# Optimization experiments

Measured on AMD Instinct MI355X. Metric: run time of the kernel, lower is better.

Reference implementation:

```python
import jax, jax.numpy as jnp
import numpy as np

KERNEL = 3
DILATIONS = (2, 3)
NUM_HEADS = 8


def _unfold_windows(t, k, dil):
    # t: [B, C, H, W] -> [B, C, k*k, H, W], same layout as nn.Unfold(k, dil, pad=dil*(k-1)//2)
    B, C, H, W = t.shape
    pad = dil * (k - 1) // 2
    tp = jnp.pad(t, ((0, 0), (0, 0), (pad, pad), (pad, pad)))
    ws = [tp[:, :, i * dil:i * dil + H, j * dil:j * dil + W]
          for i in range(k) for j in range(k)]
    return jnp.stack(ws, axis=2)


def _dilate_attention(q, k_, v, kernel, dil, head_dim):
    # q,k_,v: [B, d, H, W]
    B, d, H, W = q.shape
    nh = d // head_dim
    scale = head_dim ** (-0.5)
    qh = q.reshape(B, nh, head_dim, H, W)
    kw = _unfold_windows(k_, kernel, dil).reshape(B, nh, head_dim, kernel * kernel, H, W)
    vw = _unfold_windows(v, kernel, dil).reshape(B, nh, head_dim, kernel * kernel, H, W)
    attn = jax.nn.softmax(jnp.einsum('bndhw,bndkhw->bnkhw', qh, kw) * scale, axis=2)
    out = jnp.einsum('bnkhw,bndkhw->bndhw', attn, vw)  # [B, nh, hd, H, W]
    return out.transpose(0, 3, 4, 1, 2).reshape(B, H, W, d)


def setup_inputs() -> dict:
    key = jax.random.key(0)
    k1, k2, k3, k4 = jax.random.split(key, 4)
    B, H, W, C = 4, 128, 128, 256
    x = jax.random.normal(k1, (B, H, W, C), dtype=jnp.float32)
    Wqkv = jax.random.normal(k2, (3 * C, C), dtype=jnp.float32) * (C ** -0.5)
    Wproj = jax.random.normal(k3, (C, C), dtype=jnp.float32) * (C ** -0.5)
    bproj = jnp.zeros((C,), dtype=jnp.float32)
    return {"x": x, "Wqkv": Wqkv, "Wproj": Wproj, "bproj": bproj}


def reference(x, Wqkv, Wproj, bproj):
    B, H, W, C = x.shape
    nd = len(DILATIONS)
    head_dim = C // NUM_HEADS
    # 1x1 conv qkv (no bias), then split into 3 and nd dilation groups
    qkv = jnp.einsum('bhwc,oc->bohw', x, Wqkv).reshape(B, 3, nd, C // nd, H, W)
    outs = []
    for i, dil in enumerate(DILATIONS):
        q, k_, v = qkv[:, 0, i], qkv[:, 1, i], qkv[:, 2, i]
        outs.append(_dilate_attention(q, k_, v, KERNEL, dil, head_dim))
    xo = jnp.concatenate(outs, axis=-1)  # [B, H, W, C], dilation-group-major channels
    return jnp.einsum('bhwc,oc->bhwo', xo, Wproj) + bproj
```

## Files before the change

### kernel.cpp

```cpp
#include <hip/hip_runtime.h>
#include <stdint.h>


typedef __attribute__((ext_vector_type(8))) short bf16x8;
typedef __attribute__((ext_vector_type(4))) float f32x4;
typedef __attribute__((ext_vector_type(2))) float f32x2;

__device__ __forceinline__ f32x2 up2(unsigned u) {
  union { unsigned u; float f; } a, b;
  a.u = u << 16;
  b.u = u & 0xffff0000u;
  return (f32x2){a.f, b.f};
}
__device__ __forceinline__ unsigned short f2bf(float f) {
  union { float f; unsigned u; } x; x.f = f;
  unsigned r = x.u + 0x7fffu + ((x.u >> 16) & 1u);
  return (unsigned short)(r >> 16);
}
__device__ __forceinline__ unsigned pk2bf(float a, float b) {
  return (unsigned)f2bf(a) | ((unsigned)f2bf(b) << 16);
}

__global__ __launch_bounds__(256) void cvt_f32_to_bf16(
    const float* __restrict__ src, unsigned short* __restrict__ dst, int n) {
  int i = (blockIdx.x * 256 + threadIdx.x) * 8;
  if (i + 8 <= n) {
    const float4* s = (const float4*)(src + i);
    float4 a = s[0], b = s[1];
    uint4 o;
    o.x = pk2bf(a.x, a.y); o.y = pk2bf(a.z, a.w);
    o.z = pk2bf(b.x, b.y); o.w = pk2bf(b.z, b.w);
    *(uint4*)(dst + i) = o;
  } else {
    for (; i < n; ++i) dst[i] = f2bf(src[i]);
  }
}

__global__ __launch_bounds__(256) void cvt_w_both(
    const float* __restrict__ wqkv, const float* __restrict__ wproj,
    unsigned short* __restrict__ dst) {
  const int i = (blockIdx.x * 256 + threadIdx.x) * 8;
  const float* src = (i < 196608) ? (wqkv + i) : (wproj + (i - 196608));
  const float4* s = (const float4*)src;
  float4 a = s[0], b = s[1];
  uint4 o;
  o.x = pk2bf(a.x, a.y); o.y = pk2bf(a.z, a.w);
  o.z = pk2bf(b.x, b.y); o.w = pk2bf(b.z, b.w);
  *(uint4*)(dst + i) = o;
}

#define BARX()                                                \
  do {                                                        \
    asm volatile("s_waitcnt lgkmcnt(0)" ::: "memory");        \
    __builtin_amdgcn_s_barrier();                             \
    __builtin_amdgcn_sched_barrier(0);                        \
  } while (0)
#define WAITVM(n)                                             \
  do {                                                        \
    asm volatile("s_waitcnt vmcnt(" #n ")" ::: "memory");     \
    __builtin_amdgcn_sched_barrier(0);                        \
  } while (0)

template <int OUTF32>
__global__ __launch_bounds__(256) void gemm_bt(
    const unsigned short* __restrict__ A, const unsigned short* __restrict__ B,
    void* __restrict__ Cout, const float* __restrict__ bias,
    int N, int NT) {
  __shared__ __align__(16) unsigned short lds[3 * 8192];

  const int tid  = threadIdx.x;
  const int lane = tid & 63;
  const int wv   = tid >> 6;
  const int wr   = wv >> 1;
  const int wc   = wv & 1;

  const int nwg = gridDim.x;
  const int q8  = nwg >> 3;
  const int nid = (blockIdx.x & 7) * q8 + (blockIdx.x >> 3);
  const int n0  = (nid % NT) * 128;
  const int m0  = (nid / NT) * 128;

  const int stg_row = wv * 16 + (lane >> 2);
  const int stg_k   = ((lane & 3) ^ ((lane >> 3) & 3)) * 8;
  const unsigned short* Ag = A + (size_t)(m0 + stg_row) * 256 + stg_k;
  const unsigned short* Bg = B + (size_t)(n0 + stg_row) * 256 + stg_k;

  f32x4 acc[4][4];
#pragma unroll
  for (int i = 0; i < 4; ++i)
#pragma unroll
    for (int j = 0; j < 4; ++j) acc[i][j] = (f32x4){0.f, 0.f, 0.f, 0.f};

  const int a_r = lane & 15;

#define STAGE(buf, kt)                                                         \
  do {                                                                         \
    const unsigned short* Asrc = Ag + (kt) * 32;                               \
    const unsigned short* Bsrc = Bg + (kt) * 32;                               \
    _Pragma("unroll")                                                          \
    for (int it = 0; it < 2; ++it) {                                           \
      __builtin_amdgcn_global_load_lds(                                        \
          (const __attribute__((address_space(1))) void*)(Asrc + (size_t)it * 64 * 256), \
          (__attribute__((address_space(3))) void*)&lds[(buf) * 8192 + it * 2048 + wv * 512], \
          16, 0, 0);                                                           \
      __builtin_amdgcn_global_load_lds(                                        \
          (const __attribute__((address_space(1))) void*)(Bsrc + (size_t)it * 64 * 256), \
          (__attribute__((address_space(3))) void*)&lds[(buf) * 8192 + 4096 + it * 2048 + wv * 512], \
          16, 0, 0);                                                           \
    }                                                                          \
  } while (0)

#define COMPUTE(buf)                                                           \
  do {                                                                         \
    const int gsw = (((lane >> 4) ^ ((lane >> 1) & 3))) * 8;                   \
    bf16x8 af[4], bfr[4];                                                      \
    _Pragma("unroll")                                                          \
    for (int mi = 0; mi < 4; ++mi)                                             \
      af[mi] = *(const bf16x8*)&lds[(buf) * 8192 + (wr * 64 + mi * 16 + a_r) * 32 + gsw]; \
    _Pragma("unroll")                                                          \
    for (int ni = 0; ni < 4; ++ni)                                             \
      bfr[ni] = *(const bf16x8*)&lds[(buf) * 8192 + 4096 + (wc * 64 + ni * 16 + a_r) * 32 + gsw]; \
    _Pragma("unroll")                                                          \
    for (int mi = 0; mi < 4; ++mi)                                             \
      _Pragma("unroll")                                                        \
      for (int ni = 0; ni < 4; ++ni)                                           \
        acc[mi][ni] = __builtin_amdgcn_mfma_f32_16x16x32_bf16(                 \
            af[mi], bfr[ni], acc[mi][ni], 0, 0, 0);                            \
  } while (0)

  STAGE(0, 0);
  STAGE(1, 1);
  WAITVM(4); BARX();
  COMPUTE(0); STAGE(2, 2); WAITVM(4); BARX();
  COMPUTE(1); STAGE(0, 3); WAITVM(4); BARX();
  COMPUTE(2); STAGE(1, 4); WAITVM(4); BARX();
  COMPUTE(0); STAGE(2, 5); WAITVM(4); BARX();
  COMPUTE(1); STAGE(0, 6); WAITVM(4); BARX();
  COMPUTE(2); STAGE(1, 7); WAITVM(4); BARX();
  COMPUTE(0); WAITVM(0);   BARX();
  COMPUTE(1); BARX();

  const int cl = wc * 64 + a_r;
  const int rl = wr * 64 + (lane >> 4) * 4;
  if (!OUTF32) {
    unsigned short* eb = &lds[0];
#pragma unroll
    for (int ni = 0; ni < 4; ++ni)
#pragma unroll
      for (int mi = 0; mi < 4; ++mi)
#pragma unroll
        for (int r = 0; r < 4; ++r)
          eb[(rl + mi * 16 + r) * 136 + cl + ni * 16] = f2bf(acc[mi][ni][r]);
    BARX();
    unsigned short* C = (unsigned short*)Cout;
#pragma unroll
    for (int p = 0; p < 8; ++p) {
      const int idx = p * 256 + tid;
      const int row = idx >> 4;
      const int seg = idx & 15;
      uint4 v = *(const uint4*)&eb[row * 136 + seg * 8];
      *(uint4*)&C[(size_t)(m0 + row) * N + n0 + seg * 8] = v;
    }
  } else {
    float* ef = (float*)&lds[0];
    float* C = (float*)Cout;
    float bv[4];
#pragma unroll
    for (int ni = 0; ni < 4; ++ni) bv[ni] = bias[n0 + wc * 64 + ni * 16 + a_r];
#pragma unroll
    for (int half = 0; half < 2; ++half) {
      if (wr == half) {
        const int rb = (lane >> 4) * 4;
#pragma unroll
        for (int ni = 0; ni < 4; ++ni)
#pragma unroll
          for (int mi = 0; mi < 4; ++mi)
#pragma unroll
            for (int r = 0; r < 4; ++r)
              ef[(rb + mi * 16 + r) * 132 + wc * 64 + ni * 16 + a_r] =
                  acc[mi][ni][r] + bv[ni];
      }
      BARX();
#pragma unroll
      for (int p = 0; p < 8; ++p) {
        const int idx = p * 256 + tid;
        const int row = idx >> 5;
        const int seg = idx & 31;
        f32x4 v = *(const f32x4*)&ef[row * 132 + seg * 4];
        *(f32x4*)&C[(size_t)(m0 + half * 64 + row) * N + n0 + seg * 4] = v;
      }
      BARX();
    }
  }
#undef STAGE
#undef COMPUTE
}

__global__ __launch_bounds__(512) void attn_kernel(
    const unsigned short* __restrict__ qkv, unsigned short* __restrict__ xo) {
  __shared__ __align__(16) unsigned short lds[4 * 485 * 8];

  const int nwg = gridDim.x;
  const int q8  = nwg >> 3;
  const int nid = (blockIdx.x & 7) * q8 + (blockIdx.x >> 3);
  const int combo = nid & 7;
  const int tw    = (nid >> 3) & 7;
  const int th    = (nid >> 6) & 7;
  const int b     = nid >> 9;
  const int d     = (combo >> 2) ? 3 : 2;
  const int choff = combo * 32;
  const int h0 = th * 16, w0 = tw * 16;
  const int t = threadIdx.x;

  const int splane = t & 3;
  const int t4     = t >> 2;
  const int schoff = choff + splane * 8;

#pragma unroll
  for (int it = 0; it < 4; ++it) {
    const int px = it * 128 + t4;
    const int r = px / 22, c = px % 22;
    const int gh = h0 - d + r;
    const int gw = w0 - d + c;
    const bool ok = ((unsigned)gh < 128u) && ((unsigned)gw < 128u);
    const int hcl = min(max(gh, 0), 127);
    const int wcl = min(max(gw, 0), 127);
    const int gp = (((b << 7) | hcl) << 7) | wcl;
    uint4 u = *(const uint4*)(qkv + (size_t)gp * 768 + 256 + schoff);
    if (!ok) u = make_uint4(0u, 0u, 0u, 0u);
    if (it < 3 || t < 400) *(uint4*)&lds[(splane * 485 + px) * 8] = u;
  }

  const int half = t & 1;
  const int ph = (t >> 1) >> 4, pw = (t >> 1) & 15;
  const int gp0 = (((b << 7) | (h0 + ph)) << 7) | (w0 + pw);
  const unsigned short* qp = qkv + (size_t)gp0 * 768 + choff + half * 16;
  uint4 uq0 = *(const uint4*)qp;
  uint4 uq1 = *(const uint4*)(qp + 8);
  f32x2 q2[8];
  {
    const f32x2 s2 = {0.17677669529663687f, 0.17677669529663687f};
    q2[0] = up2(uq0.x) * s2; q2[1] = up2(uq0.y) * s2;
    q2[2] = up2(uq0.z) * s2; q2[3] = up2(uq0.w) * s2;
    q2[4] = up2(uq1.x) * s2; q2[5] = up2(uq1.y) * s2;
    q2[6] = up2(uq1.z) * s2; q2[7] = up2(uq1.w) * s2;
  }
  __syncthreads();

  const int p0 = 2 * half, p1 = 2 * half + 1;
  float sc[9];
#pragma unroll
  for (int i = 0; i < 3; ++i) {
#pragma unroll
    for (int j = 0; j < 3; ++j) {
      const int lp = (ph + i * d) * 22 + (pw + j * d);
      const uint4 k0 = *(const uint4*)&lds[(p0 * 485 + lp) * 8];
      const uint4 k1 = *(const uint4*)&lds[(p1 * 485 + lp) * 8];
      f32x2 a = q2[0] * up2(k0.x);
      a += q2[1] * up2(k0.y); a += q2[2] * up2(k0.z); a += q2[3] * up2(k0.w);
      a += q2[4] * up2(k1.x); a += q2[5] * up2(k1.y);
      a += q2[6] * up2(k1.z); a += q2[7] * up2(k1.w);
      sc[i * 3 + j] = a.x + a.y;
    }
  }
#pragma unroll
  for (int k = 0; k < 9; ++k) sc[k] += __shfl_xor(sc[k], 1);

  float mx = sc[0];
#pragma unroll
  for (int k = 1; k < 9; ++k) mx = fmaxf(mx, sc[k]);
  float sum = 0.f;
#pragma unroll
  for (int k = 0; k < 9; ++k) { sc[k] = __expf(sc[k] - mx); sum += sc[k]; }
  const float inv = 1.f / sum;

  __syncthreads();
#pragma unroll
  for (int it = 0; it < 4; ++it) {
    const int px = it * 128 + t4;
    const int r = px / 22, c = px % 22;
    const int gh = h0 - d + r;
    const int gw = w0 - d + c;
    const bool ok = ((unsigned)gh < 128u) && ((unsigned)gw < 128u);
    const int hcl = min(max(gh, 0), 127);
    const int wcl = min(max(gw, 0), 127);
    const int gp = (((b << 7) | hcl) << 7) | wcl;
    uint4 u = *(const uint4*)(qkv + (size_t)gp * 768 + 512 + schoff);
    if (!ok) u = make_uint4(0u, 0u, 0u, 0u);
    if (it < 3 || t < 400) *(uint4*)&lds[(splane * 485 + px) * 8] = u;
  }
  __syncthreads();

  f32x2 o2[8];
#pragma unroll
  for (int k = 0; k < 8; ++k) o2[k] = (f32x2){0.f, 0.f};
#pragma unroll
  for (int i = 0; i < 3; ++i) {
#pragma unroll
    for (int j = 0; j < 3; ++j) {
      const int lp = (ph + i * d) * 22 + (pw + j * d);
      const uint4 v0 = *(const uint4*)&lds[(p0 * 485 + lp) * 8];
      const uint4 v1 = *(const uint4*)&lds[(p1 * 485 + lp) * 8];
      const float wv = sc[i * 3 + j] * inv;
      const f32x2 w2 = {wv, wv};
      o2[0] += w2 * up2(v0.x); o2[1] += w2 * up2(v0.y);
      o2[2] += w2 * up2(v0.z); o2[3] += w2 * up2(v0.w);
      o2[4] += w2 * up2(v1.x); o2[5] += w2 * up2(v1.y);
      o2[6] += w2 * up2(v1.z); o2[7] += w2 * up2(v1.w);
    }
  }

  unsigned short* op = xo + (size_t)gp0 * 256 + choff + half * 16;
  uint4 s0, s1;
  s0.x = pk2bf(o2[0].x, o2[0].y); s0.y = pk2bf(o2[1].x, o2[1].y);
  s0.z = pk2bf(o2[2].x, o2[2].y); s0.w = pk2bf(o2[3].x, o2[3].y);
  s1.x = pk2bf(o2[4].x, o2[4].y); s1.y = pk2bf(o2[5].x, o2[5].y);
  s1.z = pk2bf(o2[6].x, o2[6].y); s1.w = pk2bf(o2[7].x, o2[7].y);
  *(uint4*)op       = s0;
  *(uint4*)(op + 8) = s1;
}

extern "C" void kernel_launch(void* const* d_in, const int* in_sizes, int n_in,
                              void* d_out, int out_size, void* d_ws, size_t ws_size,
                              hipStream_t stream) {
  const float* x     = (const float*)d_in[0];
  const float* Wqkv  = (const float*)d_in[1];
  const float* Wproj = (const float*)d_in[2];
  const float* bproj = (const float*)d_in[3];

  const int M = 4 * 128 * 128;
  const int C = 256;

  unsigned short* xb     = (unsigned short*)d_ws;
  unsigned short* qkvb   = xb + (size_t)M * C;
  unsigned short* xob    = qkvb + (size_t)M * 3 * C;
  unsigned short* wqkvb  = xob + (size_t)M * C;
  unsigned short* wprojb = wqkvb + (size_t)3 * C * C;

  cvt_f32_to_bf16<<<(M * C / 8 + 255) / 256, 256, 0, stream>>>(x, xb, M * C);
  cvt_w_both<<<128, 256, 0, stream>>>(Wqkv, Wproj, wqkvb);

  gemm_bt<0><<<(M / 128) * (3 * C / 128), 256, 0, stream>>>(
      xb, wqkvb, (void*)qkvb, nullptr, 3 * C, 3 * C / 128);

  attn_kernel<<<2048, 512, 0, stream>>>(qkvb, xob);

  gemm_bt<1><<<(M / 128) * (C / 128), 256, 0, stream>>>(
      xob, wprojb, d_out, bproj, C, C / 128);
}
```

Baseline: 115.8 us.

## Fuse fp32-to-bf16 input conversion into QKV GEMM A-operand staging

```diff
diff --git a/kernel.cpp b/kernel.cpp
--- a/kernel.cpp
+++ b/kernel.cpp
@@ -20,20 +20,10 @@
 __device__ __forceinline__ unsigned pk2bf(float a, float b) {
   return (unsigned)f2bf(a) | ((unsigned)f2bf(b) << 16);
 }
-
-__global__ __launch_bounds__(256) void cvt_f32_to_bf16(
-    const float* __restrict__ src, unsigned short* __restrict__ dst, int n) {
-  int i = (blockIdx.x * 256 + threadIdx.x) * 8;
-  if (i + 8 <= n) {
-    const float4* s = (const float4*)(src + i);
-    float4 a = s[0], b = s[1];
-    uint4 o;
-    o.x = pk2bf(a.x, a.y); o.y = pk2bf(a.z, a.w);
-    o.z = pk2bf(b.x, b.y); o.w = pk2bf(b.z, b.w);
-    *(uint4*)(dst + i) = o;
-  } else {
-    for (; i < n; ++i) dst[i] = f2bf(src[i]);
-  }
+__device__ __forceinline__ unsigned cvtpk(float a, float b) {
+  unsigned r;
+  asm("v_cvt_pk_bf16_f32 %0, %1, %2" : "=v"(r) : "v"(a), "v"(b));
+  return r;
 }
 
 __global__ __launch_bounds__(256) void cvt_w_both(
@@ -61,12 +51,12 @@
     __builtin_amdgcn_sched_barrier(0);                        \
   } while (0)
 
-template <int OUTF32>
+template <int OUTF32, int AF32>
 __global__ __launch_bounds__(256) void gemm_bt(
-    const unsigned short* __restrict__ A, const unsigned short* __restrict__ B,
+    const void* __restrict__ Ap, const unsigned short* __restrict__ B,
     void* __restrict__ Cout, const float* __restrict__ bias,
     int N, int NT) {
-  __shared__ __align__(16) unsigned short lds[3 * 8192];
+  __shared__ __align__(16) unsigned short lds[24576];
 
   const int tid  = threadIdx.x;
   const int lane = tid & 63;
@@ -80,10 +70,17 @@
   const int n0  = (nid % NT) * 128;
   const int m0  = (nid / NT) * 128;
 
-  const int stg_row = wv * 16 + (lane >> 2);
-  const int stg_k   = ((lane & 3) ^ ((lane >> 3) & 3)) * 8;
-  const unsigned short* Ag = A + (size_t)(m0 + stg_row) * 256 + stg_k;
-  const unsigned short* Bg = B + (size_t)(n0 + stg_row) * 256 + stg_k;
+  const float* Af          = (const float*)Ap;
+  const unsigned short* Ab = (const unsigned short*)Ap;
+
+  const int stg_rowB = wv * 16 + (lane >> 2);
+  const int stg_kB   = ((lane & 3) ^ ((lane >> 3) & 3)) * 8;
+  const unsigned short* Bg   = B  + (size_t)(n0 + stg_rowB) * 256 + stg_kB;
+  const unsigned short* Ag16 = Ab + (size_t)(m0 + stg_rowB) * 256 + stg_kB;
+
+  const int stg_rowA32 = wv * 8 + (lane >> 3);
+  const int stg_kA32   = ((lane & 7) ^ (lane >> 3)) * 4;
+  const float* Ag32 = Af + (size_t)(m0 + stg_rowA32) * 256 + stg_kA32;
 
   f32x4 acc[4][4];
 #pragma unroll
@@ -93,9 +90,9 @@
 
   const int a_r = lane & 15;
 
-#define STAGE(buf, kt)                                                         \
+#define STAGE16(buf, kt)                                                       \
   do {                                                                         \
-    const unsigned short* Asrc = Ag + (kt) * 32;                               \
+    const unsigned short* Asrc = Ag16 + (kt) * 32;                             \
     const unsigned short* Bsrc = Bg + (kt) * 32;                               \
     _Pragma("unroll")                                                          \
     for (int it = 0; it < 2; ++it) {                                           \
@@ -110,7 +107,7 @@
     }                                                                          \
   } while (0)
 
-#define COMPUTE(buf)                                                           \
+#define COMPUTE16(buf)                                                         \
   do {                                                                         \
     const int gsw = (((lane >> 4) ^ ((lane >> 1) & 3))) * 8;                   \
     bf16x8 af[4], bfr[4];                                                      \
@@ -128,17 +125,84 @@
             af[mi], bfr[ni], acc[mi][ni], 0, 0, 0);                            \
   } while (0)
 
-  STAGE(0, 0);
-  STAGE(1, 1);
-  WAITVM(4); BARX();
-  COMPUTE(0); STAGE(2, 2); WAITVM(4); BARX();
-  COMPUTE(1); STAGE(0, 3); WAITVM(4); BARX();
-  COMPUTE(2); STAGE(1, 4); WAITVM(4); BARX();
-  COMPUTE(0); STAGE(2, 5); WAITVM(4); BARX();
-  COMPUTE(1); STAGE(0, 6); WAITVM(4); BARX();
-  COMPUTE(2); STAGE(1, 7); WAITVM(4); BARX();
-  COMPUTE(0); WAITVM(0);   BARX();
-  COMPUTE(1); BARX();
+#define STAGE32(buf, kt)                                                       \
+  do {                                                                         \
+    const float* Asrc = Ag32 + (kt) * 32;                                      \
+    const unsigned short* Bsrc = Bg + (kt) * 32;                               \
+    _Pragma("unroll")                                                          \
+    for (int it = 0; it < 4; ++it)                                             \
+      __builtin_amdgcn_global_load_lds(                                        \
+          (const __attribute__((address_space(1))) void*)(Asrc + (size_t)it * 32 * 256), \
+          (__attribute__((address_space(3))) void*)&lds[(buf) * 12288 + it * 2048 + wv * 512], \
+          16, 0, 0);                                                           \
+    _Pragma("unroll")                                                          \
+    for (int it = 0; it < 2; ++it)                                             \
+      __builtin_amdgcn_global_load_lds(                                        \
+          (const __attribute__((address_space(1))) void*)(Bsrc + (size_t)it * 64 * 256), \
+          (__attribute__((address_space(3))) void*)&lds[(buf) * 12288 + 8192 + it * 2048 + wv * 512], \
+          16, 0, 0);                                                           \
+  } while (0)
+
+#define COMPUTE32(buf)                                                         \
+  do {                                                                         \
+    const int gswB = (((lane >> 4) ^ ((lane >> 1) & 3))) * 8;                  \
+    const int sA0  = ((2 * (lane >> 4)) ^ (lane & 7)) * 4;                     \
+    const int sA1  = (((2 * (lane >> 4)) ^ (lane & 7)) ^ 1) * 4;               \
+    const float* Afl = (const float*)lds;                                      \
+    bf16x8 af[4], bfr[4];                                                      \
+    _Pragma("unroll")                                                          \
+    for (int mi = 0; mi < 4; ++mi) {                                           \
+      const int rb = (buf) * 6144 + (wr * 64 + mi * 16 + a_r) * 32;            \
+      f32x4 lo = *(const f32x4*)&Afl[rb + sA0];                                \
+      f32x4 hi = *(const f32x4*)&Afl[rb + sA1];                                \
+      uint4 pk;                                                                \
+      pk.x = cvtpk(lo.x, lo.y); pk.y = cvtpk(lo.z, lo.w);                      \
+      pk.z = cvtpk(hi.x, hi.y); pk.w = cvtpk(hi.z, hi.w);                      \
+      af[mi] = *(bf16x8*)&pk;                                                  \
+    }                                                                          \
+    _Pragma("unroll")                                                          \
+    for (int ni = 0; ni < 4; ++ni)                                             \
+      bfr[ni] = *(const bf16x8*)&lds[(buf) * 12288 + 8192 + (wc * 64 + ni * 16 + a_r) * 32 + gswB]; \
+    _Pragma("unroll")                                                          \
+    for (int mi = 0; mi < 4; ++mi)                                             \
+      _Pragma("unroll")                                                        \
+      for (int ni = 0; ni < 4; ++ni)                                           \
+        acc[mi][ni] = __builtin_amdgcn_mfma_f32_16x16x32_bf16(                 \
+            af[mi], bfr[ni], acc[mi][ni], 0, 0, 0);                            \
+  } while (0)
+
+  if constexpr (AF32) {
+    STAGE32(0, 0);
+    STAGE32(1, 1);
+    WAITVM(6);  BARX();
+    COMPUTE32(0); BARX();
+    STAGE32(0, 2); WAITVM(6); BARX();
+    COMPUTE32(1); BARX();
+    STAGE32(1, 3); WAITVM(6); BARX();
+    COMPUTE32(0); BARX();
+    STAGE32(0, 4); WAITVM(6); BARX();
+    COMPUTE32(1); BARX();
+    STAGE32(1, 5); WAITVM(6); BARX();
+    COMPUTE32(0); BARX();
+    STAGE32(0, 6); WAITVM(6); BARX();
+    COMPUTE32(1); BARX();
+    STAGE32(1, 7); WAITVM(6); BARX();
+    COMPUTE32(0); BARX();
+    WAITVM(0);   BARX();
+    COMPUTE32(1); BARX();
+  } else {
+    STAGE16(0, 0);
+    STAGE16(1, 1);
+    WAITVM(4); BARX();
+    COMPUTE16(0); STAGE16(2, 2); WAITVM(4); BARX();
+    COMPUTE16(1); STAGE16(0, 3); WAITVM(4); BARX();
+    COMPUTE16(2); STAGE16(1, 4); WAITVM(4); BARX();
+    COMPUTE16(0); STAGE16(2, 5); WAITVM(4); BARX();
+    COMPUTE16(1); STAGE16(0, 6); WAITVM(4); BARX();
+    COMPUTE16(2); STAGE16(1, 7); WAITVM(4); BARX();
+    COMPUTE16(0); WAITVM(0);   BARX();
+    COMPUTE16(1); BARX();
+  }
 
   const int cl = wc * 64 + a_r;
   const int rl = wr * 64 + (lane >> 4) * 4;
@@ -192,8 +256,10 @@
       BARX();
     }
   }
-#undef STAGE
-#undef COMPUTE
+#undef STAGE16
+#undef COMPUTE16
+#undef STAGE32
+#undef COMPUTE32
 }
 
 __global__ __launch_bounds__(512) void attn_kernel(
@@ -331,20 +397,19 @@
   const int M = 4 * 128 * 128;
   const int C = 256;
 
-  unsigned short* xb     = (unsigned short*)d_ws;
-  unsigned short* qkvb   = xb + (size_t)M * C;
+  unsigned short* qkvb   = (unsigned short*)d_ws;
   unsigned short* xob    = qkvb + (size_t)M * 3 * C;
   unsigned short* wqkvb  = xob + (size_t)M * C;
   unsigned short* wprojb = wqkvb + (size_t)3 * C * C;
-
-  cvt_f32_to_bf16<<<(M * C / 8 + 255) / 256, 256, 0, stream>>>(x, xb, M * C);
+  (void)wprojb;
+
   cvt_w_both<<<128, 256, 0, stream>>>(Wqkv, Wproj, wqkvb);
 
-  gemm_bt<0><<<(M / 128) * (3 * C / 128), 256, 0, stream>>>(
-      xb, wqkvb, (void*)qkvb, nullptr, 3 * C, 3 * C / 128);
+  gemm_bt<0, 1><<<(M / 128) * (3 * C / 128), 256, 0, stream>>>(
+      (const void*)x, wqkvb, (void*)qkvb, nullptr, 3 * C, 3 * C / 128);
 
   attn_kernel<<<2048, 512, 0, stream>>>(qkvb, xob);
 
-  gemm_bt<1><<<(M / 128) * (C / 128), 256, 0, stream>>>(
-      xob, wprojb, d_out, bproj, C, C / 128);
-}
+  gemm_bt<1, 0><<<(M / 128) * (C / 128), 256, 0, stream>>>(
+      (const void*)xob, wqkvb + (size_t)3 * C * C, d_out, bproj, C, C / 128);
+}
```

Result: faster. 110.7 us (-4.4%).

## Fuse x fp32-to-bf16 conversion into the QKV GEMM A-operand load path

Applied to the files above, without the earlier changes.

```diff
diff --git a/kernel.cpp b/kernel.cpp
--- a/kernel.cpp
+++ b/kernel.cpp
@@ -20,20 +20,10 @@
 __device__ __forceinline__ unsigned pk2bf(float a, float b) {
   return (unsigned)f2bf(a) | ((unsigned)f2bf(b) << 16);
 }
-
-__global__ __launch_bounds__(256) void cvt_f32_to_bf16(
-    const float* __restrict__ src, unsigned short* __restrict__ dst, int n) {
-  int i = (blockIdx.x * 256 + threadIdx.x) * 8;
-  if (i + 8 <= n) {
-    const float4* s = (const float4*)(src + i);
-    float4 a = s[0], b = s[1];
-    uint4 o;
-    o.x = pk2bf(a.x, a.y); o.y = pk2bf(a.z, a.w);
-    o.z = pk2bf(b.x, b.y); o.w = pk2bf(b.z, b.w);
-    *(uint4*)(dst + i) = o;
-  } else {
-    for (; i < n; ++i) dst[i] = f2bf(src[i]);
-  }
+__device__ __forceinline__ unsigned cvtpk(float a, float b) {
+  unsigned r;
+  asm("v_cvt_pk_bf16_f32 %0, %1, %2" : "=v"(r) : "v"(a), "v"(b));
+  return r;
 }
 
 __global__ __launch_bounds__(256) void cvt_w_both(
@@ -61,9 +51,9 @@
     __builtin_amdgcn_sched_barrier(0);                        \
   } while (0)
 
-template <int OUTF32>
+template <int OUTF32, int AF32>
 __global__ __launch_bounds__(256) void gemm_bt(
-    const unsigned short* __restrict__ A, const unsigned short* __restrict__ B,
+    const void* __restrict__ Ap, const unsigned short* __restrict__ B,
     void* __restrict__ Cout, const float* __restrict__ bias,
     int N, int NT) {
   __shared__ __align__(16) unsigned short lds[3 * 8192];
@@ -80,10 +70,20 @@
   const int n0  = (nid % NT) * 128;
   const int m0  = (nid / NT) * 128;
 
-  const int stg_row = wv * 16 + (lane >> 2);
-  const int stg_k   = ((lane & 3) ^ ((lane >> 3) & 3)) * 8;
-  const unsigned short* Ag = A + (size_t)(m0 + stg_row) * 256 + stg_k;
-  const unsigned short* Bg = B + (size_t)(n0 + stg_row) * 256 + stg_k;
+  const float* Af          = (const float*)Ap;
+  const unsigned short* Ab = (const unsigned short*)Ap;
+
+  const int stg_rowB = wv * 16 + (lane >> 2);
+  const int stg_kB   = ((lane & 3) ^ ((lane >> 3) & 3)) * 8;
+  const unsigned short* Bg   = B  + (size_t)(n0 + stg_rowB) * 256 + stg_kB;
+  const unsigned short* Ag16 = Ab + (size_t)(m0 + stg_rowB) * 256 + stg_kB;
+
+  const int arow  = tid >> 1;
+  const int akh   = tid & 1;
+  const int akey  = (arow >> 1) & 3;
+  const int aoff0 = (((2 * akh) ^ akey)) * 8;
+  const int aoff1 = (((2 * akh + 1) ^ akey)) * 8;
+  const float* Axg = Af + (size_t)(m0 + arow) * 256 + akh * 16;
 
   f32x4 acc[4][4];
 #pragma unroll
@@ -93,21 +93,45 @@
 
   const int a_r = lane & 15;
 
-#define STAGE(buf, kt)                                                         \
-  do {                                                                         \
-    const unsigned short* Asrc = Ag + (kt) * 32;                               \
+#define STAGE_B(buf, kt)                                                       \
+  do {                                                                         \
     const unsigned short* Bsrc = Bg + (kt) * 32;                               \
     _Pragma("unroll")                                                          \
-    for (int it = 0; it < 2; ++it) {                                           \
+    for (int it = 0; it < 2; ++it)                                             \
+      __builtin_amdgcn_global_load_lds(                                        \
+          (const __attribute__((address_space(1))) void*)(Bsrc + (size_t)it * 64 * 256), \
+          (__attribute__((address_space(3))) void*)&lds[(buf) * 8192 + 4096 + it * 2048 + wv * 512], \
+          16, 0, 0);                                                           \
+  } while (0)
+
+#define STAGE_A16(buf, kt)                                                     \
+  do {                                                                         \
+    const unsigned short* Asrc = Ag16 + (kt) * 32;                             \
+    _Pragma("unroll")                                                          \
+    for (int it = 0; it < 2; ++it)                                             \
       __builtin_amdgcn_global_load_lds(                                        \
           (const __attribute__((address_space(1))) void*)(Asrc + (size_t)it * 64 * 256), \
           (__attribute__((address_space(3))) void*)&lds[(buf) * 8192 + it * 2048 + wv * 512], \
           16, 0, 0);                                                           \
-      __builtin_amdgcn_global_load_lds(                                        \
-          (const __attribute__((address_space(1))) void*)(Bsrc + (size_t)it * 64 * 256), \
-          (__attribute__((address_space(3))) void*)&lds[(buf) * 8192 + 4096 + it * 2048 + wv * 512], \
-          16, 0, 0);                                                           \
-    }                                                                          \
+  } while (0)
+
+#define ISSUE_A(dst, kt)                                                       \
+  do {                                                                         \
+    dst[0] = *(const f32x4*)(Axg + (kt) * 32 + 0);                             \
+    dst[1] = *(const f32x4*)(Axg + (kt) * 32 + 4);                             \
+    dst[2] = *(const f32x4*)(Axg + (kt) * 32 + 8);                             \
+    dst[3] = *(const f32x4*)(Axg + (kt) * 32 + 12);                            \
+  } while (0)
+
+#define WRITE_A(src, buf)                                                      \
+  do {                                                                         \
+    uint4 p0, p1;                                                              \
+    p0.x = cvtpk(src[0].x, src[0].y); p0.y = cvtpk(src[0].z, src[0].w);        \
+    p0.z = cvtpk(src[1].x, src[1].y); p0.w = cvtpk(src[1].z, src[1].w);        \
+    p1.x = cvtpk(src[2].x, src[2].y); p1.y = cvtpk(src[2].z, src[2].w);        \
+    p1.z = cvtpk(src[3].x, src[3].y); p1.w = cvtpk(src[3].z, src[3].w);        \
+    *(uint4*)&lds[(buf) * 8192 + arow * 32 + aoff0] = p0;                      \
+    *(uint4*)&lds[(buf) * 8192 + arow * 32 + aoff1] = p1;                      \
   } while (0)
 
 #define COMPUTE(buf)                                                           \
@@ -128,17 +152,34 @@
             af[mi], bfr[ni], acc[mi][ni], 0, 0, 0);                            \
   } while (0)
 
-  STAGE(0, 0);
-  STAGE(1, 1);
-  WAITVM(4); BARX();
-  COMPUTE(0); STAGE(2, 2); WAITVM(4); BARX();
-  COMPUTE(1); STAGE(0, 3); WAITVM(4); BARX();
-  COMPUTE(2); STAGE(1, 4); WAITVM(4); BARX();
-  COMPUTE(0); STAGE(2, 5); WAITVM(4); BARX();
-  COMPUTE(1); STAGE(0, 6); WAITVM(4); BARX();
-  COMPUTE(2); STAGE(1, 7); WAITVM(4); BARX();
-  COMPUTE(0); WAITVM(0);   BARX();
-  COMPUTE(1); BARX();
+  if constexpr (AF32) {
+    f32x4 rAa[4], rAb[4];
+    ISSUE_A(rAa, 0); STAGE_B(0, 0);
+    ISSUE_A(rAb, 1); STAGE_B(1, 1);
+    WAITVM(6);
+    WRITE_A(rAa, 0);
+    BARX();
+    COMPUTE(0); ISSUE_A(rAa, 2); STAGE_B(2, 2); WAITVM(6); WRITE_A(rAb, 1); BARX();
+    COMPUTE(1); ISSUE_A(rAb, 3); STAGE_B(0, 3); WAITVM(6); WRITE_A(rAa, 2); BARX();
+    COMPUTE(2); ISSUE_A(rAa, 4); STAGE_B(1, 4); WAITVM(6); WRITE_A(rAb, 0); BARX();
+    COMPUTE(0); ISSUE_A(rAb, 5); STAGE_B(2, 5); WAITVM(6); WRITE_A(rAa, 1); BARX();
+    COMPUTE(1); ISSUE_A(rAa, 6); STAGE_B(0, 6); WAITVM(6); WRITE_A(rAb, 2); BARX();
+    COMPUTE(2); ISSUE_A(rAb, 7); STAGE_B(1, 7); WAITVM(6); WRITE_A(rAa, 0); BARX();
+    COMPUTE(0); WAITVM(0); WRITE_A(rAb, 1); BARX();
+    COMPUTE(1); BARX();
+  } else {
+    STAGE_A16(0, 0); STAGE_B(0, 0);
+    STAGE_A16(1, 1); STAGE_B(1, 1);
+    WAITVM(4); BARX();
+    COMPUTE(0); STAGE_A16(2, 2); STAGE_B(2, 2); WAITVM(4); BARX();
+    COMPUTE(1); STAGE_A16(0, 3); STAGE_B(0, 3); WAITVM(4); BARX();
+    COMPUTE(2); STAGE_A16(1, 4); STAGE_B(1, 4); WAITVM(4); BARX();
+    COMPUTE(0); STAGE_A16(2, 5); STAGE_B(2, 5); WAITVM(4); BARX();
+    COMPUTE(1); STAGE_A16(0, 6); STAGE_B(0, 6); WAITVM(4); BARX();
+    COMPUTE(2); STAGE_A16(1, 7); STAGE_B(1, 7); WAITVM(4); BARX();
+    COMPUTE(0); WAITVM(0); BARX();
+    COMPUTE(1); BARX();
+  }
 
   const int cl = wc * 64 + a_r;
   const int rl = wr * 64 + (lane >> 4) * 4;
@@ -192,7 +233,10 @@
       BARX();
     }
   }
-#undef STAGE
+#undef STAGE_B
+#undef STAGE_A16
+#undef ISSUE_A
+#undef WRITE_A
 #undef COMPUTE
 }
 
@@ -331,20 +375,17 @@
   const int M = 4 * 128 * 128;
   const int C = 256;
 
-  unsigned short* xb     = (unsigned short*)d_ws;
-  unsigned short* qkvb   = xb + (size_t)M * C;
+  unsigned short* qkvb   = (unsigned short*)d_ws;
   unsigned short* xob    = qkvb + (size_t)M * 3 * C;
   unsigned short* wqkvb  = xob + (size_t)M * C;
-  unsigned short* wprojb = wqkvb + (size_t)3 * C * C;
-
-  cvt_f32_to_bf16<<<(M * C / 8 + 255) / 256, 256, 0, stream>>>(x, xb, M * C);
+
   cvt_w_both<<<128, 256, 0, stream>>>(Wqkv, Wproj, wqkvb);
 
-  gemm_bt<0><<<(M / 128) * (3 * C / 128), 256, 0, stream>>>(
-      xb, wqkvb, (void*)qkvb, nullptr, 3 * C, 3 * C / 128);
+  gemm_bt<0, 1><<<(M / 128) * (3 * C / 128), 256, 0, stream>>>(
+      (const void*)x, wqkvb, (void*)qkvb, nullptr, 3 * C, 3 * C / 128);
 
   attn_kernel<<<2048, 512, 0, stream>>>(qkvb, xob);
 
-  gemm_bt<1><<<(M / 128) * (C / 128), 256, 0, stream>>>(
-      xob, wprojb, d_out, bproj, C, C / 128);
-}
+  gemm_bt<1, 0><<<(M / 128) * (C / 128), 256, 0, stream>>>(
+      (const void*)xob, wqkvb + (size_t)3 * C * C, d_out, bproj, C, C / 128);
+}
```

Measured after the change: 114.3 us, median of 5. About the same (-1.2%).
